# Performance work log

Hardware: AMD Instinct MI355X
Metric: run time of the kernel (lower is better)

Reference implementation:

```python
import jax, jax.numpy as jnp
import numpy as np


def setup_inputs() -> dict:
    key = jax.random.key(0)
    ks = jax.random.split(key, 6)
    B, N, D_in, D, Dg, H = 32, 256, 512, 256, 256, 512
    s = lambda f_in: 1.0 / np.sqrt(f_in)
    return {
        "xi": jax.random.normal(ks[0], (B, N, D_in), dtype=jnp.float32),
        "W_img": jax.random.normal(ks[1], (D_in, D), dtype=jnp.float32) * s(D_in),
        "b_img": jnp.zeros((D,), jnp.float32),
        "W_gnn_self": jax.random.normal(ks[2], (D, Dg), dtype=jnp.float32) * s(D),
        "W_gnn_nbr": jax.random.normal(ks[3], (D, Dg), dtype=jnp.float32) * s(D),
        "b_gnn": jnp.zeros((Dg,), jnp.float32),
        "W1": jax.random.normal(ks[4], (N * Dg, H), dtype=jnp.float32) * s(N * Dg),
        "b1": jnp.zeros((H,), jnp.float32),
        "W2": jax.random.normal(ks[5], (H, 1), dtype=jnp.float32) * s(H),
        "b2": jnp.zeros((1,), jnp.float32),
        "k": 10,
    }


def _knn_edges(xie, k):
    # xie: [B, N, D]. Per-image squared euclidean cdist + top-k (exclude self).
    B, N, _ = xie.shape
    x2 = jnp.sum(xie * xie, axis=-1)  # [B, N]
    d2 = x2[:, :, None] + x2[:, None, :] - 2.0 * jnp.einsum("bnd,bmd->bnm", xie, xie)
    big = jnp.asarray(1e30, d2.dtype)
    d2 = d2 + big * jnp.eye(N, dtype=d2.dtype)  # exclude self
    _, nbr = jax.lax.top_k(-d2, k)  # [B, N, k] neighbor (source) indices
    tgt = jnp.broadcast_to(jnp.arange(N)[None, :, None], (B, N, k))
    return nbr, tgt


def reference(xi, W_img, b_img, W_gnn_self, W_gnn_nbr, b_gnn, W1, b1, W2, b2, k):
    B, N, _ = xi.shape
    # image encoder -> per-node embeddings [B, N, D]
    xie = xi @ W_img + b_img
    # KNN graph build per image, then shift indices into one batched graph
    nbr, tgt = _knn_edges(xie, k)
    shift = (jnp.arange(B) * N)[:, None, None]
    src = (nbr + shift).reshape(-1)  # [B*N*k]
    dst = (tgt + shift).reshape(-1)  # [B*N*k]
    # batched graph conv: mean neighbor aggregation + self transform
    x_flat = xie.reshape(B * N, -1)
    agg = jax.ops.segment_sum(x_flat[src], dst, num_segments=B * N) / k
    gep = jax.nn.relu(x_flat @ W_gnn_self + agg @ W_gnn_nbr + b_gnn)
    gep = gep.reshape(B, N, -1)  # split_batch_graph
    # estimation MLP on flattened graph embedding
    h = jax.nn.relu(gep.reshape(B, -1) @ W1 + b1)
    out = h @ W2 + b2  # [B, 1]
    return xie, gep, out
```

## Files before the change

### kernel.cpp

```cpp
#include <hip/hip_runtime.h>

#define BB 32
#define NN 256
#define DIN 512
#define DD 256
#define HH 512
#define MM 8192
#define KSTR 16

typedef __attribute__((ext_vector_type(8))) __bf16 bf16x8;
typedef __attribute__((ext_vector_type(4))) float f32x4;
typedef unsigned short ushort_t;

typedef const float __attribute__((address_space(1)))* gas1f;
typedef const unsigned int __attribute__((address_space(1)))* gas1u;
typedef unsigned int __attribute__((address_space(3)))* las3u;

__device__ __forceinline__ unsigned short f2bf(float x) {
  unsigned u = __float_as_uint(x);
  u += 0x7FFFu + ((u >> 16) & 1u);
  return (unsigned short)(u >> 16);
}

__global__ __launch_bounds__(512) void k_enc(const float* __restrict__ A,
                                             const float* __restrict__ W,
                                             const float* __restrict__ bias,
                                             float* __restrict__ C,
                                             ushort_t* __restrict__ A_bf,
                                             float* __restrict__ xieT,
                                             float* __restrict__ x2g) {
  __shared__ float Asm[32][520];
  const int tid = threadIdx.x;
  const int mb0 = blockIdx.x * 32;
  const int cg = tid & 31;
  const int mh = (tid >> 5) & 7;
  const int team = tid >> 8;
#pragma unroll
  for (int i = 0; i < 8; ++i) {
    int idx = tid + i * 512;
    int m = idx >> 7;
    int kq = idx & 127;
    float4 v = *reinterpret_cast<const float4*>(&A[(size_t)(mb0 + m) * DIN + kq * 4]);
    *reinterpret_cast<float4*>(&Asm[m][kq * 4]) = v;
  }
  __syncthreads();
  float4 acc[4][2] = {};
  const int kt0 = team * 256;
  const float* wp = &W[(size_t)kt0 * DD + cg * 8];
  float4 wA[4][2], wB[4][2];
#pragma unroll
  for (int j = 0; j < 4; ++j) {
    wA[j][0] = *reinterpret_cast<const float4*>(&wp[(size_t)j * DD]);
    wA[j][1] = *reinterpret_cast<const float4*>(&wp[(size_t)j * DD + 4]);
  }
  for (int it = 0; it < 64; ++it) {
    if (it < 63) {
#pragma unroll
      for (int j = 0; j < 4; ++j) {
        wB[j][0] = *reinterpret_cast<const float4*>(&wp[(size_t)((it + 1) * 4 + j) * DD]);
        wB[j][1] = *reinterpret_cast<const float4*>(&wp[(size_t)((it + 1) * 4 + j) * DD + 4]);
      }
    }
    const int kk = kt0 + it * 4;
#pragma unroll
    for (int r = 0; r < 4; ++r) {
      float4 a = *reinterpret_cast<const float4*>(&Asm[mh * 4 + r][kk]);
#pragma unroll
      for (int h = 0; h < 2; ++h) {
        acc[r][h].x += a.x * wA[0][h].x; acc[r][h].y += a.x * wA[0][h].y;
        acc[r][h].z += a.x * wA[0][h].z; acc[r][h].w += a.x * wA[0][h].w;
        acc[r][h].x += a.y * wA[1][h].x; acc[r][h].y += a.y * wA[1][h].y;
        acc[r][h].z += a.y * wA[1][h].z; acc[r][h].w += a.y * wA[1][h].w;
        acc[r][h].x += a.z * wA[2][h].x; acc[r][h].y += a.z * wA[2][h].y;
        acc[r][h].z += a.z * wA[2][h].z; acc[r][h].w += a.z * wA[2][h].w;
        acc[r][h].x += a.w * wA[3][h].x; acc[r][h].y += a.w * wA[3][h].y;
        acc[r][h].z += a.w * wA[3][h].z; acc[r][h].w += a.w * wA[3][h].w;
      }
    }
#pragma unroll
    for (int j = 0; j < 4; ++j) {
      wA[j][0] = wB[j][0]; wA[j][1] = wB[j][1];
    }
  }
  __syncthreads();
  float* red = &Asm[0][0];
  if (team == 1) {
#pragma unroll
    for (int r = 0; r < 4; ++r) {
      *reinterpret_cast<float4*>(&red[(mh * 4 + r) * 256 + cg * 8]) = acc[r][0];
      *reinterpret_cast<float4*>(&red[(mh * 4 + r) * 256 + cg * 8 + 4]) = acc[r][1];
    }
  }
  __syncthreads();
  if (team == 0) {
    float4 bv0 = *reinterpret_cast<const float4*>(&bias[cg * 8]);
    float4 bv1 = *reinterpret_cast<const float4*>(&bias[cg * 8 + 4]);
#pragma unroll
    for (int r = 0; r < 4; ++r) {
      const int row = mb0 + mh * 4 + r;
      float4 o0 = *reinterpret_cast<float4*>(&red[(mh * 4 + r) * 256 + cg * 8]);
      float4 o1 = *reinterpret_cast<float4*>(&red[(mh * 4 + r) * 256 + cg * 8 + 4]);
      float4 s0, s1;
      s0.x = acc[r][0].x + o0.x + bv0.x; s0.y = acc[r][0].y + o0.y + bv0.y;
      s0.z = acc[r][0].z + o0.z + bv0.z; s0.w = acc[r][0].w + o0.w + bv0.w;
      s1.x = acc[r][1].x + o1.x + bv1.x; s1.y = acc[r][1].y + o1.y + bv1.y;
      s1.z = acc[r][1].z + o1.z + bv1.z; s1.w = acc[r][1].w + o1.w + bv1.w;
      *reinterpret_cast<float4*>(&C[(size_t)row * DD + cg * 8]) = s0;
      *reinterpret_cast<float4*>(&C[(size_t)row * DD + cg * 8 + 4]) = s1;
      ushort4 ob0, ob1;
      ob0.x = f2bf(s0.x); ob0.y = f2bf(s0.y); ob0.z = f2bf(s0.z); ob0.w = f2bf(s0.w);
      ob1.x = f2bf(s1.x); ob1.y = f2bf(s1.y); ob1.z = f2bf(s1.z); ob1.w = f2bf(s1.w);
      *reinterpret_cast<ushort4*>(&A_bf[(size_t)row * 512 + cg * 8]) = ob0;
      *reinterpret_cast<ushort4*>(&A_bf[(size_t)row * 512 + cg * 8 + 4]) = ob1;
      *reinterpret_cast<float4*>(&red[(mh * 4 + r) * 256 + cg * 8]) = s0;
      *reinterpret_cast<float4*>(&red[(mh * 4 + r) * 256 + cg * 8 + 4]) = s1;
    }
  }
  __syncthreads();
  {
    const int lane = tid & 63;
    const int w8 = tid >> 6;
#pragma unroll
    for (int rr = 0; rr < 4; ++rr) {
      const int row = w8 * 4 + rr;
      float4 v = *reinterpret_cast<const float4*>(&red[row * 256 + lane * 4]);
      float s = v.x * v.x + v.y * v.y + v.z * v.z + v.w * v.w;
#pragma unroll
      for (int off = 1; off < 64; off <<= 1) s += __shfl_xor(s, off);
      if (lane == 0) x2g[mb0 + row] = s;
    }
  }
  {
    const int b = mb0 >> 8;
    const int n0b = mb0 & 255;
    const int d = tid >> 1;
    const int nh = (tid & 1) * 16;
    float tmp[16];
#pragma unroll
    for (int i = 0; i < 16; ++i) tmp[i] = red[(nh + i) * 256 + d];
    float* dst = &xieT[((size_t)b * 256 + d) * 256 + n0b + nh];
#pragma unroll
    for (int i = 0; i < 4; ++i)
      *reinterpret_cast<float4*>(&dst[i * 4]) = *reinterpret_cast<float4*>(&tmp[i * 4]);
  }
}

__global__ __launch_bounds__(512) void k_dist(const float* __restrict__ xie,
                                              const float* __restrict__ xieT,
                                              const float* __restrict__ x2g,
                                              float* __restrict__ d2,
                                              const float* __restrict__ Ws,
                                              const float* __restrict__ Wn,
                                              ushort_t* __restrict__ B_bfT) {
  __shared__ float Asm[32][260];
  const int tid = threadIdx.x;
  const int b = blockIdx.x >> 3;
  const int n0b = (blockIdx.x & 7) * 32;
  const int base = b * 256;
  const int cg = tid & 31;
  const int rg = tid >> 5;
#pragma unroll
  for (int i = 0; i < 4; ++i) {
    int idx = tid + i * 512;
    int m = idx >> 6;
    int kq = idx & 63;
    float4 v = *reinterpret_cast<const float4*>(
        &xie[(size_t)(base + n0b + m) * DD + kq * 4]);
    *reinterpret_cast<float4*>(&Asm[m][kq * 4]) = v;
  }
  __syncthreads();
  float4 acc[2][2] = {};
  const float* wp = &xieT[(size_t)base * 256 + cg * 8];
  float4 wA[4][2], wB[4][2];
#pragma unroll
  for (int j = 0; j < 4; ++j) {
    wA[j][0] = *reinterpret_cast<const float4*>(&wp[(size_t)j * 256]);
    wA[j][1] = *reinterpret_cast<const float4*>(&wp[(size_t)j * 256 + 4]);
  }
  for (int it = 0; it < 64; ++it) {
    if (it < 63) {
#pragma unroll
      for (int j = 0; j < 4; ++j) {
        wB[j][0] = *reinterpret_cast<const float4*>(&wp[(size_t)((it + 1) * 4 + j) * 256]);
        wB[j][1] = *reinterpret_cast<const float4*>(&wp[(size_t)((it + 1) * 4 + j) * 256 + 4]);
      }
    }
#pragma unroll
    for (int r = 0; r < 2; ++r) {
      float4 a = *reinterpret_cast<const float4*>(&Asm[rg * 2 + r][it * 4]);
#pragma unroll
      for (int h = 0; h < 2; ++h) {
        acc[r][h].x += a.x * wA[0][h].x; acc[r][h].y += a.x * wA[0][h].y;
        acc[r][h].z += a.x * wA[0][h].z; acc[r][h].w += a.x * wA[0][h].w;
        acc[r][h].x += a.y * wA[1][h].x; acc[r][h].y += a.y * wA[1][h].y;
        acc[r][h].z += a.y * wA[1][h].z; acc[r][h].w += a.y * wA[1][h].w;
        acc[r][h].x += a.z * wA[2][h].x; acc[r][h].y += a.z * wA[2][h].y;
        acc[r][h].z += a.z * wA[2][h].z; acc[r][h].w += a.z * wA[2][h].w;
        acc[r][h].x += a.w * wA[3][h].x; acc[r][h].y += a.w * wA[3][h].y;
        acc[r][h].z += a.w * wA[3][h].z; acc[r][h].w += a.w * wA[3][h].w;
      }
    }
#pragma unroll
    for (int j = 0; j < 4; ++j) {
      wA[j][0] = wB[j][0]; wA[j][1] = wB[j][1];
    }
  }
#pragma unroll
  for (int r = 0; r < 2; ++r) {
    const int nl = n0b + rg * 2 + r;
    const float xn = x2g[base + nl];
#pragma unroll
    for (int h = 0; h < 2; ++h) {
      const float* accp = reinterpret_cast<const float*>(&acc[r][h]);
      float4 v;
      float* vv = reinterpret_cast<float*>(&v);
#pragma unroll
      for (int j2 = 0; j2 < 4; ++j2) {
        const int mc = cg * 8 + h * 4 + j2;
        float dv = xn + x2g[base + mc] - 2.0f * accp[j2];
        if (nl == mc) dv = 1e30f;
        vv[j2] = dv;
      }
      *reinterpret_cast<float4*>(&d2[(size_t)(base + nl) * 256 + cg * 8 + h * 4]) = v;
    }
  }
  {
    const int id = blockIdx.x * 512 + tid;
    const int k = id >> 8;
    const int n = id & 255;
    float v = (k < 256) ? Ws[(size_t)k * 256 + n] : Wn[(size_t)(k - 256) * 256 + n];
    B_bfT[(size_t)n * 512 + k] = f2bf(v);
  }
}

__global__ __launch_bounds__(256) void k_topkagg(const float* __restrict__ X,
                                                 const float* __restrict__ d2,
                                                 const int* __restrict__ kp,
                                                 ushort_t* __restrict__ A_bf) {
  __shared__ int nbrL[4][KSTR];
  const int tid = threadIdx.x;
  const int rw = tid >> 6;
  const int i = blockIdx.x * 4 + rw;
  const int lane = tid & 63;
  const int kcnt = kp[0];
  const float* row = d2 + (size_t)i * NN;
  float v0 = row[lane];
  float v1 = row[lane + 64];
  float v2 = row[lane + 128];
  float v3 = row[lane + 192];
  for (int it = 0; it < kcnt; ++it) {
    float v = v0; int idx = lane;
    if (v1 < v) { v = v1; idx = lane + 64; }
    if (v2 < v) { v = v2; idx = lane + 128; }
    if (v3 < v) { v = v3; idx = lane + 192; }
#pragma unroll
    for (int off = 1; off < 64; off <<= 1) {
      float ov = __shfl_xor(v, off);
      int oi = __shfl_xor(idx, off);
      if (ov < v || (ov == v && oi < idx)) { v = ov; idx = oi; }
    }
    if (lane == 0) nbrL[rw][it] = idx;
    const int slot = idx >> 6;
    if (lane == (idx & 63)) {
      if (slot == 0) v0 = 3e38f;
      else if (slot == 1) v1 = 3e38f;
      else if (slot == 2) v2 = 3e38f;
      else v3 = 3e38f;
    }
  }
  __syncthreads();
  {
    const int b = i >> 8;
    float4 s = make_float4(0.f, 0.f, 0.f, 0.f);
    for (int j = 0; j < kcnt; ++j) {
      const int nb = nbrL[rw][j];
      float4 v = *reinterpret_cast<const float4*>(
          &X[(size_t)(b * NN + nb) * DD + lane * 4]);
      s.x += v.x; s.y += v.y; s.z += v.z; s.w += v.w;
    }
    const float sc = 1.0f / (float)kcnt;
    ushort4 ob;
    ob.x = f2bf(s.x * sc); ob.y = f2bf(s.y * sc);
    ob.z = f2bf(s.z * sc); ob.w = f2bf(s.w * sc);
    *reinterpret_cast<ushort4*>(&A_bf[(size_t)i * 512 + 256 + lane * 4]) = ob;
  }
}

__global__ __launch_bounds__(256) void k_gnn(const ushort_t* __restrict__ A_bf,
                                             const ushort_t* __restrict__ B_bfT,
                                             const float* __restrict__ bias,
                                             float* __restrict__ C,
                                             ushort_t* __restrict__ gep_bf) {
  __shared__ ushort_t As[64 * 72];
  __shared__ ushort_t Bs[64 * 72];
  const int tid = threadIdx.x;
  const int m0 = blockIdx.x * 64, n0 = blockIdx.y * 64;
  const int l = tid & 63, w = tid >> 6;
  const int mw = (w & 1) * 32, nw = (w >> 1) * 32;
  const int lr = tid >> 3, lq = tid & 7;
  f32x4 acc[2][2] = {};
  for (int kt = 0; kt < 8; ++kt) {
    const int kb = kt * 64;
#pragma unroll
    for (int s = 0; s < 2; ++s) {
      const int r = lr + s * 32;
      uint4 va = *reinterpret_cast<const uint4*>(&A_bf[(size_t)(m0 + r) * 512 + kb + lq * 8]);
      *reinterpret_cast<uint4*>(&As[r * 72 + lq * 8]) = va;
      uint4 vb = *reinterpret_cast<const uint4*>(&B_bfT[(size_t)(n0 + r) * 512 + kb + lq * 8]);
      *reinterpret_cast<uint4*>(&Bs[r * 72 + lq * 8]) = vb;
    }
    __syncthreads();
#pragma unroll
    for (int ks = 0; ks < 2; ++ks) {
      bf16x8 af[2], bf[2];
#pragma unroll
      for (int mi = 0; mi < 2; ++mi)
        af[mi] = *reinterpret_cast<const bf16x8*>(
            &As[(mw + mi * 16 + (l & 15)) * 72 + ks * 32 + (l >> 4) * 8]);
#pragma unroll
      for (int ni = 0; ni < 2; ++ni)
        bf[ni] = *reinterpret_cast<const bf16x8*>(
            &Bs[(nw + ni * 16 + (l & 15)) * 72 + ks * 32 + (l >> 4) * 8]);
#pragma unroll
      for (int mi = 0; mi < 2; ++mi)
#pragma unroll
        for (int ni = 0; ni < 2; ++ni)
          acc[mi][ni] = __builtin_amdgcn_mfma_f32_16x16x32_bf16(af[mi], bf[ni],
                                                                acc[mi][ni], 0, 0, 0);
    }
    __syncthreads();
  }
#pragma unroll
  for (int mi = 0; mi < 2; ++mi) {
    const int row_base = m0 + mw + mi * 16 + (l >> 4) * 4;
#pragma unroll
    for (int ni = 0; ni < 2; ++ni) {
      const int col = n0 + nw + ni * 16 + (l & 15);
      const float bv = bias[col];
#pragma unroll
      for (int r = 0; r < 4; ++r) {
        float v = acc[mi][ni][r] + bv;
        v = v > 0.0f ? v : 0.0f;
        C[(size_t)(row_base + r) * 256 + col] = v;
        gep_bf[(size_t)(row_base + r) * 256 + col] = f2bf(v);
      }
    }
  }
}

__global__ __launch_bounds__(512) void k_mlp1(const ushort_t* __restrict__ gep_bf,
                                              const float* __restrict__ W1,
                                              float* __restrict__ part) {
  __shared__ ushort_t WbT[2][512][40];
  __shared__ ushort_t Ab[32][264];
  const int tid = threadIdx.x;
  const int b = blockIdx.x;
  const int l = tid & 63, w = tid >> 6;
#pragma unroll
  for (int i = 0; i < 2; ++i) {
    int id = tid + i * 512;
    int m = id >> 5, dq8 = (id & 31) * 8;
    *reinterpret_cast<uint4*>(&Ab[m][dq8]) = *reinterpret_cast<const uint4*>(
        &gep_bf[((size_t)m * 256 + b) * 256 + dq8]);
  }
  const float* Wbase = W1 + (size_t)b * 256 * 512 + tid;
  float wreg[32];
  auto WLOAD = [&](int s) {
#pragma unroll
    for (int kk = 0; kk < 32; ++kk)
      wreg[kk] = Wbase[(size_t)(s * 32 + kk) * 512];
  };
  auto WSTORE = [&](int buf) {
#pragma unroll
    for (int q = 0; q < 4; ++q) {
      ushort_t tmp[8];
#pragma unroll
      for (int j = 0; j < 8; ++j) tmp[j] = f2bf(wreg[q * 8 + j]);
      *reinterpret_cast<uint4*>(&WbT[buf][tid][q * 8]) =
          *reinterpret_cast<const uint4*>(tmp);
    }
  };
  WLOAD(0);
  WSTORE(0);
  __syncthreads();
  const int n0w = w * 64;
  f32x4 acc[2][4] = {};
  for (int s = 0; s < 8; ++s) {
    const int cur = s & 1;
    if (s < 7) WLOAD(s + 1);
    bf16x8 a[2], bw[4];
#pragma unroll
    for (int mi = 0; mi < 2; ++mi)
      a[mi] = *reinterpret_cast<const bf16x8*>(
          &Ab[mi * 16 + (l & 15)][s * 32 + (l >> 4) * 8]);
#pragma unroll
    for (int nf = 0; nf < 4; ++nf)
      bw[nf] = *reinterpret_cast<const bf16x8*>(
          &WbT[cur][n0w + nf * 16 + (l & 15)][(l >> 4) * 8]);
#pragma unroll
    for (int mi = 0; mi < 2; ++mi)
#pragma unroll
      for (int nf = 0; nf < 4; ++nf)
        acc[mi][nf] = __builtin_amdgcn_mfma_f32_16x16x32_bf16(a[mi], bw[nf],
                                                              acc[mi][nf], 0, 0, 0);
    if (s < 7) {
      WSTORE(cur ^ 1);
      __syncthreads();
    }
  }
#pragma unroll
  for (int mi = 0; mi < 2; ++mi)
#pragma unroll
    for (int nf = 0; nf < 4; ++nf) {
      const int col = n0w + nf * 16 + (l & 15);
#pragma unroll
      for (int r = 0; r < 4; ++r) {
        const int m = mi * 16 + (l >> 4) * 4 + r;
        part[((size_t)b * 32 + m) * HH + col] = acc[mi][nf][r];
      }
    }
}

__global__ __launch_bounds__(256) void k_hred(const float* __restrict__ part,
                                              float* __restrict__ hpart) {
  const int tid = threadIdx.x;
  const int m = blockIdx.x >> 3;
  const int s = blockIdx.x & 7;
  const int c0 = tid * 2;
  float a0 = 0.f, a1 = 0.f;
  for (int bb = s * 32; bb < s * 32 + 32; ++bb) {
    float2 v = *reinterpret_cast<const float2*>(&part[((size_t)bb * 32 + m) * 512 + c0]);
    a0 += v.x; a1 += v.y;
  }
  float2 o; o.x = a0; o.y = a1;
  *reinterpret_cast<float2*>(&hpart[((size_t)s * 32 + m) * 512 + c0]) = o;
}

__global__ __launch_bounds__(256) void k_out2(const float* __restrict__ hpart,
                                              const float* __restrict__ b1,
                                              const float* __restrict__ W2,
                                              const float* __restrict__ b2,
                                              float* __restrict__ outp) {
  __shared__ float red[4];
  const int tid = threadIdx.x;
  const int m = blockIdx.x;
  const int c0 = tid * 2;
  float a0 = 0.f, a1 = 0.f;
#pragma unroll
  for (int s = 0; s < 8; ++s) {
    float2 v = *reinterpret_cast<const float2*>(&hpart[((size_t)s * 32 + m) * 512 + c0]);
    a0 += v.x; a1 += v.y;
  }
  float h0 = a0 + b1[c0];
  float h1 = a1 + b1[c0 + 1];
  h0 = h0 > 0.f ? h0 : 0.f;
  h1 = h1 > 0.f ? h1 : 0.f;
  float val = h0 * W2[c0] + h1 * W2[c0 + 1];
#pragma unroll
  for (int off = 1; off < 64; off <<= 1) val += __shfl_xor(val, off);
  const int w = tid >> 6;
  if ((tid & 63) == 0) red[w] = val;
  __syncthreads();
  if (tid == 0) outp[m] = red[0] + red[1] + red[2] + red[3] + b2[0];
}

extern "C" void kernel_launch(void* const* d_in, const int* in_sizes, int n_in,
                              void* d_out, int out_size, void* d_ws, size_t ws_size,
                              hipStream_t stream) {
  const float* xi     = (const float*)d_in[0];
  const float* W_img  = (const float*)d_in[1];
  const float* b_img  = (const float*)d_in[2];
  const float* W_self = (const float*)d_in[3];
  const float* W_nbr  = (const float*)d_in[4];
  const float* b_gnn  = (const float*)d_in[5];
  const float* W1     = (const float*)d_in[6];
  const float* b1     = (const float*)d_in[7];
  const float* W2     = (const float*)d_in[8];
  const float* b2     = (const float*)d_in[9];
  const int*   kp     = (const int*)d_in[10];

  float* xie  = (float*)d_out;
  float* gep  = xie + (size_t)MM * DD;
  float* outp = gep + (size_t)MM * DD;

  float* ws   = (float*)d_ws;
  float* x2   = ws;
  float* d2   = ws + 8192;
  float* part = d2 + (size_t)2097152;
  float* xieT = part + (size_t)4194304;
  float* hpart = xieT + (size_t)2097152;
  ushort_t* A_bf   = (ushort_t*)(hpart + 131072);
  ushort_t* B_bfT  = A_bf + (size_t)MM * 512;
  ushort_t* gep_bf = B_bfT + 131072;

  k_enc    <<<MM / 32, 512, 0, stream>>>(xi, W_img, b_img, xie, A_bf, xieT, x2);
  k_dist   <<<256, 512, 0, stream>>>(xie, xieT, x2, d2, W_self, W_nbr, B_bfT);
  k_topkagg<<<MM / 4, 256, 0, stream>>>(xie, d2, kp, A_bf);
  k_gnn    <<<dim3(128, 4), 256, 0, stream>>>(A_bf, B_bfT, b_gnn, gep, gep_bf);
  k_mlp1   <<<256, 512, 0, stream>>>(gep_bf, W1, part);
  k_hred   <<<256, 256, 0, stream>>>(part, hpart);
  k_out2   <<<BB, 256, 0, stream>>>(hpart, b1, W2, b2, outp);
}
```

Before: 136.2 us.

## Fuse top-k selection and neighbor aggregation into the distance kernel

The distance kernel now keeps each 32x256 distance tile in registers, runs the k-nearest selection with 32-lane shuffle reductions, and averages the neighbor embeddings directly into the bf16 activation buffer. This removes the separate top-k/aggregation launch and the 8 MB d2 round trip through global memory. In exchange, the 256-block distance kernel now does the serial top-k loop at low parallelism (each 32-lane group handles two rows in sequence), which could lengthen that kernel's critical path.

```diff
diff --git a/kernel.cpp b/kernel.cpp
--- a/kernel.cpp
+++ b/kernel.cpp
@@ -148,17 +148,20 @@
 __global__ __launch_bounds__(512) void k_dist(const float* __restrict__ xie,
                                               const float* __restrict__ xieT,
                                               const float* __restrict__ x2g,
-                                              float* __restrict__ d2,
+                                              const int* __restrict__ kp,
+                                              ushort_t* __restrict__ A_bf,
                                               const float* __restrict__ Ws,
                                               const float* __restrict__ Wn,
                                               ushort_t* __restrict__ B_bfT) {
   __shared__ float Asm[32][260];
+  __shared__ int nbrL[32][KSTR];
   const int tid = threadIdx.x;
   const int b = blockIdx.x >> 3;
   const int n0b = (blockIdx.x & 7) * 32;
   const int base = b * 256;
   const int cg = tid & 31;
   const int rg = tid >> 5;
+  const int kcnt = kp[0];
 #pragma unroll
   for (int i = 0; i < 4; ++i) {
     int idx = tid + i * 512;
@@ -205,6 +208,7 @@
       wA[j][0] = wB[j][0]; wA[j][1] = wB[j][1];
     }
   }
+  float v[2][8];
 #pragma unroll
   for (int r = 0; r < 2; ++r) {
     const int nl = n0b + rg * 2 + r;
@@ -212,77 +216,70 @@
 #pragma unroll
     for (int h = 0; h < 2; ++h) {
       const float* accp = reinterpret_cast<const float*>(&acc[r][h]);
-      float4 v;
-      float* vv = reinterpret_cast<float*>(&v);
 #pragma unroll
       for (int j2 = 0; j2 < 4; ++j2) {
         const int mc = cg * 8 + h * 4 + j2;
         float dv = xn + x2g[base + mc] - 2.0f * accp[j2];
         if (nl == mc) dv = 1e30f;
-        vv[j2] = dv;
-      }
-      *reinterpret_cast<float4*>(&d2[(size_t)(base + nl) * 256 + cg * 8 + h * 4]) = v;
-    }
+        v[r][h * 4 + j2] = dv;
+      }
+    }
+  }
+#pragma unroll
+  for (int r = 0; r < 2; ++r) {
+    for (int it2 = 0; it2 < kcnt; ++it2) {
+      float lv = v[r][0]; int li = 0;
+#pragma unroll
+      for (int j = 1; j < 8; ++j)
+        if (v[r][j] < lv) { lv = v[r][j]; li = j; }
+      int midx = cg * 8 + li;
+#pragma unroll
+      for (int off = 1; off < 32; off <<= 1) {
+        float ov = __shfl_xor(lv, off);
+        int oi = __shfl_xor(midx, off);
+        if (ov < lv || (ov == lv && oi < midx)) { lv = ov; midx = oi; }
+      }
+      if (cg == 0) nbrL[rg * 2 + r][it2] = midx;
+      const bool mine = (cg == (midx >> 3));
+      const int jw = midx & 7;
+#pragma unroll
+      for (int j = 0; j < 8; ++j)
+        v[r][j] = (mine && j == jw) ? 3e38f : v[r][j];
+    }
+  }
+  __syncthreads();
+  {
+    const int row = tid >> 4;
+    const int q0 = (tid & 15) * 16;
+    float4 a4[4] = {};
+    for (int j = 0; j < kcnt; ++j) {
+      const int nb = nbrL[row][j];
+      const float* src = &xie[(size_t)(base + nb) * DD + q0];
+#pragma unroll
+      for (int q = 0; q < 4; ++q) {
+        float4 vv = *reinterpret_cast<const float4*>(&src[q * 4]);
+        a4[q].x += vv.x; a4[q].y += vv.y; a4[q].z += vv.z; a4[q].w += vv.w;
+      }
+    }
+    const float sc = 1.0f / (float)kcnt;
+    ushort_t ob[16];
+#pragma unroll
+    for (int q = 0; q < 4; ++q) {
+      ob[q * 4 + 0] = f2bf(a4[q].x * sc);
+      ob[q * 4 + 1] = f2bf(a4[q].y * sc);
+      ob[q * 4 + 2] = f2bf(a4[q].z * sc);
+      ob[q * 4 + 3] = f2bf(a4[q].w * sc);
+    }
+    ushort_t* dst = &A_bf[(size_t)(base + n0b + row) * 512 + 256 + q0];
+    *reinterpret_cast<uint4*>(&dst[0]) = *reinterpret_cast<uint4*>(&ob[0]);
+    *reinterpret_cast<uint4*>(&dst[8]) = *reinterpret_cast<uint4*>(&ob[8]);
   }
   {
     const int id = blockIdx.x * 512 + tid;
     const int k = id >> 8;
     const int n = id & 255;
-    float v = (k < 256) ? Ws[(size_t)k * 256 + n] : Wn[(size_t)(k - 256) * 256 + n];
-    B_bfT[(size_t)n * 512 + k] = f2bf(v);
-  }
-}
-
-__global__ __launch_bounds__(256) void k_topkagg(const float* __restrict__ X,
-                                                 const float* __restrict__ d2,
-                                                 const int* __restrict__ kp,
-                                                 ushort_t* __restrict__ A_bf) {
-  __shared__ int nbrL[4][KSTR];
-  const int tid = threadIdx.x;
-  const int rw = tid >> 6;
-  const int i = blockIdx.x * 4 + rw;
-  const int lane = tid & 63;
-  const int kcnt = kp[0];
-  const float* row = d2 + (size_t)i * NN;
-  float v0 = row[lane];
-  float v1 = row[lane + 64];
-  float v2 = row[lane + 128];
-  float v3 = row[lane + 192];
-  for (int it = 0; it < kcnt; ++it) {
-    float v = v0; int idx = lane;
-    if (v1 < v) { v = v1; idx = lane + 64; }
-    if (v2 < v) { v = v2; idx = lane + 128; }
-    if (v3 < v) { v = v3; idx = lane + 192; }
-#pragma unroll
-    for (int off = 1; off < 64; off <<= 1) {
-      float ov = __shfl_xor(v, off);
-      int oi = __shfl_xor(idx, off);
-      if (ov < v || (ov == v && oi < idx)) { v = ov; idx = oi; }
-    }
-    if (lane == 0) nbrL[rw][it] = idx;
-    const int slot = idx >> 6;
-    if (lane == (idx & 63)) {
-      if (slot == 0) v0 = 3e38f;
-      else if (slot == 1) v1 = 3e38f;
-      else if (slot == 2) v2 = 3e38f;
-      else v3 = 3e38f;
-    }
-  }
-  __syncthreads();
-  {
-    const int b = i >> 8;
-    float4 s = make_float4(0.f, 0.f, 0.f, 0.f);
-    for (int j = 0; j < kcnt; ++j) {
-      const int nb = nbrL[rw][j];
-      float4 v = *reinterpret_cast<const float4*>(
-          &X[(size_t)(b * NN + nb) * DD + lane * 4]);
-      s.x += v.x; s.y += v.y; s.z += v.z; s.w += v.w;
-    }
-    const float sc = 1.0f / (float)kcnt;
-    ushort4 ob;
-    ob.x = f2bf(s.x * sc); ob.y = f2bf(s.y * sc);
-    ob.z = f2bf(s.z * sc); ob.w = f2bf(s.w * sc);
-    *reinterpret_cast<ushort4*>(&A_bf[(size_t)i * 512 + 256 + lane * 4]) = ob;
+    float vw = (k < 256) ? Ws[(size_t)k * 256 + n] : Wn[(size_t)(k - 256) * 256 + n];
+    B_bfT[(size_t)n * 512 + k] = f2bf(vw);
   }
 }
 
@@ -485,19 +482,17 @@
 
   float* ws   = (float*)d_ws;
   float* x2   = ws;
-  float* d2   = ws + 8192;
-  float* part = d2 + (size_t)2097152;
+  float* part = ws + 8192;
   float* xieT = part + (size_t)4194304;
   float* hpart = xieT + (size_t)2097152;
   ushort_t* A_bf   = (ushort_t*)(hpart + 131072);
   ushort_t* B_bfT  = A_bf + (size_t)MM * 512;
   ushort_t* gep_bf = B_bfT + 131072;
 
-  k_enc    <<<MM / 32, 512, 0, stream>>>(xi, W_img, b_img, xie, A_bf, xieT, x2);
-  k_dist   <<<256, 512, 0, stream>>>(xie, xieT, x2, d2, W_self, W_nbr, B_bfT);
-  k_topkagg<<<MM / 4, 256, 0, stream>>>(xie, d2, kp, A_bf);
-  k_gnn    <<<dim3(128, 4), 256, 0, stream>>>(A_bf, B_bfT, b_gnn, gep, gep_bf);
-  k_mlp1   <<<256, 512, 0, stream>>>(gep_bf, W1, part);
-  k_hred   <<<256, 256, 0, stream>>>(part, hpart);
-  k_out2   <<<BB, 256, 0, stream>>>(hpart, b1, W2, b2, outp);
-}
+  k_enc  <<<MM / 32, 512, 0, stream>>>(xi, W_img, b_img, xie, A_bf, xieT, x2);
+  k_dist <<<256, 512, 0, stream>>>(xie, xieT, x2, kp, A_bf, W_self, W_nbr, B_bfT);
+  k_gnn  <<<dim3(128, 4), 256, 0, stream>>>(A_bf, B_bfT, b_gnn, gep, gep_bf);
+  k_mlp1 <<<256, 512, 0, stream>>>(gep_bf, W1, part);
+  k_hred <<<256, 256, 0, stream>>>(part, hpart);
+  k_out2 <<<BB, 256, 0, stream>>>(hpart, b1, W2, b2, outp);
+}
```

Result: no change. 135.9 us (-0.2%).
